# Kernel tuning notes

Hardware: AMD Instinct MI355X
Metric: run time of the kernel (lower is better)

Reference implementation:

```python
import jax, jax.numpy as jnp
import numpy as np

N_NODES = 50000
N_EDGES = 800000
IN_DIM = 128
HIDDEN_DIMS = [128, 128]
OUT_DIM = 4
NUM_GRAPHS = 128


def setup_inputs() -> dict:
    key = jax.random.key(0)
    ks = jax.random.split(key, 12)
    inp = {
        "x": jax.random.normal(ks[0], (N_NODES, IN_DIM), dtype=jnp.float32),
        "edge_index": jax.random.randint(ks[1], (2, N_EDGES), 0, N_NODES, dtype=jnp.int64),
        "edge_attr": jax.random.uniform(ks[2], (N_EDGES,), dtype=jnp.float32),
        "edge_weight": jax.random.uniform(ks[3], (N_EDGES,), dtype=jnp.float32),
        "batch": jnp.sort(jax.random.randint(ks[4], (N_NODES,), 0, NUM_GRAPHS, dtype=jnp.int64)),
    }
    # GCNConv weights (Glorot-ish scale) and biases
    d_in = IN_DIM
    for i, d_out in enumerate(HIDDEN_DIMS):
        inp[f"W{i}"] = jax.random.normal(ks[5 + i], (d_in, d_out), dtype=jnp.float32) / np.sqrt(d_in)
        inp[f"b{i}"] = jnp.zeros((d_out,), dtype=jnp.float32)
        d_in = d_out
    # classifier: Linear(d,d) -> ReLU -> Linear(d,4)
    inp["Wc1"] = jax.random.normal(ks[8], (d_in, d_in), dtype=jnp.float32) / np.sqrt(d_in)
    inp["bc1"] = jnp.zeros((d_in,), dtype=jnp.float32)
    inp["Wc2"] = jax.random.normal(ks[9], (d_in, OUT_DIM), dtype=jnp.float32) / np.sqrt(d_in)
    inp["bc2"] = jnp.zeros((OUT_DIM,), dtype=jnp.float32)
    return inp


def _gcn_conv(x, src, dst, ew, W, b):
    # PyG GCNConv with add_self_loops=True, symmetric normalization.
    n = x.shape[0]
    loop = jnp.arange(n, dtype=src.dtype)
    s = jnp.concatenate([src, loop])
    d = jnp.concatenate([dst, loop])
    w = jnp.concatenate([ew, jnp.ones((n,), dtype=ew.dtype)])
    deg = jax.ops.segment_sum(w, d, num_segments=n)
    dinv = jnp.where(deg > 0, jax.lax.rsqrt(jnp.maximum(deg, 1e-12)), 0.0)
    norm = dinv[s] * w * dinv[d]  # [E+N]
    h = x @ W                     # [N, d_out] dense GEMM
    out = jax.ops.segment_sum(h[s] * norm[:, None], d, num_segments=n)
    return out + b


def reference(x, edge_index, edge_attr, edge_weight, batch,
              W0, b0, W1, b1, Wc1, bc1, Wc2, bc2):
    # NOTE: original code passes edge_attr into GCNConv's edge_weight slot;
    # edge_weight is unused. Dropout is identity (eval mode).
    src, dst = edge_index[0], edge_index[1]
    h = x
    for W, b in ((W0, b0), (W1, b1)):
        h = _gcn_conv(h, src, dst, edge_attr, W, b)
        h = jax.nn.relu(h)
    # global mean pool over graphs
    sums = jax.ops.segment_sum(h, batch, num_segments=NUM_GRAPHS)
    cnts = jax.ops.segment_sum(jnp.ones((h.shape[0],), h.dtype), batch, num_segments=NUM_GRAPHS)
    g = sums / jnp.maximum(cnts, 1.0)[:, None]  # [G, d]
    # classifier MLP
    g = jax.nn.relu(g @ Wc1 + bc1)
    return g @ Wc2 + bc2  # [G, 4]
```

## Files before the change

### kernel.cpp

```cpp
#include <hip/hip_runtime.h>
#include <hip/hip_fp16.h>

#define N_NODES 50000
#define N_EDGES 800000
#define DIM 128
#define NUM_GRAPHS 128
#define STRIDE 64

#define ATTR_SCALE 33554432.0f
#define ATTR_MASK  ((1ull << 40) - 1)

typedef _Float16 f16x8 __attribute__((ext_vector_type(8)));
typedef float f32x4 __attribute__((ext_vector_type(4)));


__global__ __launch_bounds__(256) void k_zero(unsigned long long* packed,
                                              float* gz, int n) {
    int i = blockIdx.x * 256 + threadIdx.x;
    if (i < n) packed[i] = 0ull;
    if (i < NUM_GRAPHS * DIM + NUM_GRAPHS) gz[i] = 0.f;
}


__global__ __launch_bounds__(256) void k_build(const int* __restrict__ src,
                                               const int* __restrict__ dst,
                                               const float* __restrict__ attr,
                                               unsigned long long* packed,
                                               unsigned int* __restrict__ epack,
                                               int E) {
    int e = blockIdx.x * 256 + threadIdx.x;
    if (e >= E) return;
    int d = dst[e];
    float a = attr[e];
    unsigned long long add =
        (1ull << 40) | (unsigned long long)(unsigned int)(a * ATTR_SCALE + 0.5f);
    unsigned long long old = atomicAdd(&packed[d], add);
    int rank = (int)(old >> 40);
    if (rank < STRIDE) {
        __half ha = __float2half_rn(a);
        unsigned short us = *reinterpret_cast<unsigned short*>(&ha);
        epack[d * STRIDE + rank] = ((unsigned int)us << 16) | (unsigned int)src[e];
    }
}


__global__ __launch_bounds__(128) void k_prep_w(const float* __restrict__ W0,
                                                const float* __restrict__ W1,
                                                _Float16* __restrict__ Wt0,
                                                _Float16* __restrict__ Wt1) {
    int b = blockIdx.x;
    const float* W = (b & 1) ? W1 : W0;
    _Float16* Wt = (b & 1) ? Wt1 : Wt0;
    int k = b >> 1;
    int nn = threadIdx.x;
    Wt[(size_t)nn * 128 + k] = (_Float16)W[(size_t)k * 128 + nn];
}


__global__ __launch_bounds__(256) void k_gemm_mfma(const float* __restrict__ A,
                                                   const _Float16* __restrict__ Wt,
                                                   const unsigned long long* __restrict__ packed,
                                                   __half* __restrict__ H, int n) {
    int tid = threadIdx.x;
    int w = tid >> 6, lane = tid & 63;
    int n15 = lane & 15, quad = lane >> 4;
    int row = blockIdx.x * 64 + w * 16 + n15;
    int rowc = row < n ? row : n - 1;
    const float4* Arow = (const float4*)(A + (size_t)rowc * DIM);

    f32x4 acc[8];
#pragma unroll
    for (int t = 0; t < 8; t++) acc[t] = (f32x4){0.f, 0.f, 0.f, 0.f};

#pragma unroll
    for (int c = 0; c < 4; c++) {
        float4 a0 = Arow[c * 8 + quad * 2];
        float4 a1 = Arow[c * 8 + quad * 2 + 1];
        f16x8 af;
        af[0] = (_Float16)a0.x; af[1] = (_Float16)a0.y;
        af[2] = (_Float16)a0.z; af[3] = (_Float16)a0.w;
        af[4] = (_Float16)a1.x; af[5] = (_Float16)a1.y;
        af[6] = (_Float16)a1.z; af[7] = (_Float16)a1.w;
#pragma unroll
        for (int t = 0; t < 8; t++) {
            f16x8 bf = *(const f16x8*)(Wt + (size_t)(t * 16 + n15) * 128 + c * 32 + quad * 8);
            acc[t] = __builtin_amdgcn_mfma_f32_16x16x32_f16(af, bf, acc[t], 0, 0, 0);
        }
    }

    int orow0 = blockIdx.x * 64 + w * 16 + quad * 4;
#pragma unroll
    for (int r = 0; r < 4; r++) {
        int orow = orow0 + r;
        if (orow < n) {
            unsigned long long pk = packed[orow];
            float dv = rsqrtf(1.0f + (float)(pk & ATTR_MASK) * (1.0f / ATTR_SCALE));
            __half* hp = H + (size_t)orow * DIM + n15;
#pragma unroll
            for (int t = 0; t < 8; t++) hp[t * 16] = __float2half_rn(acc[t][r] * dv);
        }
    }
}


__device__ __forceinline__ float2 unpack_h2(unsigned int u) {
    __half2 h = *reinterpret_cast<__half2*>(&u);
    return __half22float2(h);
}

template <bool POOL>
__global__ __launch_bounds__(256) void k_gather(const __half* __restrict__ H,
                                                const unsigned long long* __restrict__ packed,
                                                const unsigned int* __restrict__ epack,
                                                const float* __restrict__ bias,
                                                const int* __restrict__ batch,
                                                float* __restrict__ OUT,
                                                float* gsum, float* cnt, int n) {
    __shared__ float lpool[8 * 128];
    __shared__ int sg[8];

    int idx = blockIdx.x * 256 + threadIdx.x;
    int i = idx >> 5;
    int lane = idx & 31;
    int w = threadIdx.x >> 5;
    const uint2* H8 = (const uint2*)H;

    unsigned long long pk = packed[i];
    int cntE = (int)(pk >> 40);
    if (cntE > STRIDE) cntE = STRIDE;
    float dv = rsqrtf(1.0f + (float)(pk & ATTR_MASK) * (1.0f / ATTR_SCALE));

    uint2 selfraw = H8[(size_t)i * 32 + lane];
    float2 s01 = unpack_h2(selfraw.x);
    float2 s23 = unpack_h2(selfraw.y);
    float4 acc = make_float4(s01.x, s01.y, s23.x, s23.y);

    int j0 = i * STRIDE;
    int end = j0 + cntE;

    for (int j = j0; j < end; j += 8) {
        int s[8];
        float wt[8];
#pragma unroll
        for (int k = 0; k < 8; k++) {
            int jj = j + k;
            bool valid = jj < end;
            int jc = valid ? jj : (end - 1);
            unsigned int pe = epack[jc];
            s[k] = (int)(pe & 0xffffu);
            __half_raw hr;
            hr.x = (unsigned short)(pe >> 16);
            float wv = __half2float(__half(hr));
            wt[k] = valid ? wv : 0.f;
        }
        uint2 v[8];
#pragma unroll
        for (int k = 0; k < 8; k++) v[k] = H8[(size_t)s[k] * 32 + lane];
#pragma unroll
        for (int k = 0; k < 8; k++) {
            float2 f01 = unpack_h2(v[k].x);
            float2 f23 = unpack_h2(v[k].y);
            acc.x += wt[k] * f01.x;
            acc.y += wt[k] * f01.y;
            acc.z += wt[k] * f23.x;
            acc.w += wt[k] * f23.y;
        }
    }

    float4 bb = ((const float4*)bias)[lane];
    acc.x = fmaxf(acc.x * dv + bb.x, 0.f);
    acc.y = fmaxf(acc.y * dv + bb.y, 0.f);
    acc.z = fmaxf(acc.z * dv + bb.z, 0.f);
    acc.w = fmaxf(acc.w * dv + bb.w, 0.f);

    if (POOL) {
        int g = batch[i];
        if (lane == 0) sg[w] = g;
        __syncthreads();
        bool uniform = true;
#pragma unroll
        for (int k = 0; k < 8; k++) uniform = uniform && (sg[k] == sg[0]);
        if (uniform) {
            ((float4*)(lpool + w * 128))[lane] = acc;
            __syncthreads();
            int t = threadIdx.x;
            if (t < 128) {
                float s = 0.f;
#pragma unroll
                for (int k = 0; k < 8; k++) s += lpool[k * 128 + t];
                atomicAdd(&gsum[sg[0] * DIM + t], s);
            }
            if (t == 0) atomicAdd(&cnt[sg[0]], 8.0f);
        } else {
            float* o = gsum + (size_t)g * DIM + lane * 4;
            atomicAdd(o + 0, acc.x);
            atomicAdd(o + 1, acc.y);
            atomicAdd(o + 2, acc.z);
            atomicAdd(o + 3, acc.w);
            if (lane == 0) atomicAdd(&cnt[g], 1.0f);
        }
    } else {
        ((float4*)OUT)[(size_t)i * 32 + lane] = acc;
    }
}


__global__ __launch_bounds__(128) void k_classifier(const float* __restrict__ gsum,
                                                    const float* __restrict__ cnt,
                                                    const float* __restrict__ Wc1,
                                                    const float* __restrict__ bc1,
                                                    const float* __restrict__ Wc2,
                                                    const float* __restrict__ bc2,
                                                    float* __restrict__ out) {
    int g = blockIdx.x;
    int t = threadIdx.x;
    __shared__ float gv[128];
    __shared__ float hid[128];
    float inv = 1.0f / fmaxf(cnt[g], 1.0f);
    gv[t] = gsum[(size_t)g * DIM + t] * inv;
    __syncthreads();
    float acc = bc1[t];
    for (int k = 0; k < 128; k++) acc += gv[k] * Wc1[k * 128 + t];
    hid[t] = fmaxf(acc, 0.f);
    __syncthreads();
    if (t < 4) {
        float o = bc2[t];
        for (int k = 0; k < 128; k++) o += hid[k] * Wc2[k * 4 + t];
        out[g * 4 + t] = o;
    }
}


extern "C" void kernel_launch(void* const* d_in, const int* in_sizes, int n_in,
                              void* d_out, int out_size, void* d_ws, size_t ws_size,
                              hipStream_t stream) {
    const float* x     = (const float*)d_in[0];
    const int*   ei    = (const int*)d_in[1];
    const float* attr  = (const float*)d_in[2];
    const int*   batch = (const int*)d_in[4];
    const float* W0  = (const float*)d_in[5];
    const float* b0  = (const float*)d_in[6];
    const float* W1  = (const float*)d_in[7];
    const float* b1  = (const float*)d_in[8];
    const float* Wc1 = (const float*)d_in[9];
    const float* bc1 = (const float*)d_in[10];
    const float* Wc2 = (const float*)d_in[11];
    const float* bc2 = (const float*)d_in[12];
    float* out = (float*)d_out;

    char* ws = (char*)d_ws;
    __half*             bufH16 = (__half*)(ws + 0);
    float*              bufA   = (float*)(ws + 12800000);
    unsigned int*       epack  = (unsigned int*)(ws + 38400000);
    unsigned long long* packed = (unsigned long long*)(ws + 51200000);
    float*              gsum   = (float*)(ws + 51600000);
    float*              cnt    = (float*)(ws + 51665536);
    _Float16*           Wt0    = (_Float16*)(ws + 51666048);
    _Float16*           Wt1    = (_Float16*)(ws + 51698816);

    const int* src = ei;
    const int* dst = ei + N_EDGES;

    const int NB_N = (N_NODES + 255) / 256;
    const int NB_E = (N_EDGES + 255) / 256;
    const int NB_G = (N_NODES * 32 + 255) / 256;
    const int NB_M = (N_NODES + 63) / 64;

    k_zero<<<NB_N, 256, 0, stream>>>(packed, gsum, N_NODES);
    k_prep_w<<<256, 128, 0, stream>>>(W0, W1, Wt0, Wt1);
    k_build<<<NB_E, 256, 0, stream>>>(src, dst, attr, packed, epack, N_EDGES);

    k_gemm_mfma<<<NB_M, 256, 0, stream>>>(x, Wt0, packed, bufH16, N_NODES);
    k_gather<false><<<NB_G, 256, 0, stream>>>(bufH16, packed, epack, b0,
                                              batch, bufA, gsum, cnt, N_NODES);

    k_gemm_mfma<<<NB_M, 256, 0, stream>>>(bufA, Wt1, packed, bufH16, N_NODES);
    k_gather<true><<<NB_G, 256, 0, stream>>>(bufH16, packed, epack, b1,
                                             batch, nullptr, gsum, cnt, N_NODES);

    k_classifier<<<NUM_GRAPHS, 128, 0, stream>>>(gsum, cnt, Wc1, bc1, Wc2, bc2, out);
}
```

Baseline: 278.9 us.

## Store layer-1 activations in fp16, swap MFMA operands, fuse prep kernels

The layer-1 gather output is now written as fp16, and the second GEMM reads it directly with no float-to-half conversion. This halves that intermediate's traffic. The MFMA operands are swapped so each lane holds four consecutive output columns, which allows packed 8-byte half stores in place of scattered 2-byte stores. Zeroing moves to a hipMemsetAsync, and the weight transpose is folded into extra blocks of the build kernel, cutting launch count. Layer-2 input precision drops from fp32 to fp16 before the GEMM, though the GEMM already converted it to fp16, so accuracy is essentially unchanged.

```diff
diff --git a/kernel.cpp b/kernel.cpp
--- a/kernel.cpp
+++ b/kernel.cpp
@@ -14,21 +14,29 @@
 typedef float f32x4 __attribute__((ext_vector_type(4)));
 
 
-__global__ __launch_bounds__(256) void k_zero(unsigned long long* packed,
-                                              float* gz, int n) {
-    int i = blockIdx.x * 256 + threadIdx.x;
-    if (i < n) packed[i] = 0ull;
-    if (i < NUM_GRAPHS * DIM + NUM_GRAPHS) gz[i] = 0.f;
-}
-
-
 __global__ __launch_bounds__(256) void k_build(const int* __restrict__ src,
                                                const int* __restrict__ dst,
                                                const float* __restrict__ attr,
+                                               const float* __restrict__ W0,
+                                               const float* __restrict__ W1,
                                                unsigned long long* packed,
                                                unsigned int* __restrict__ epack,
-                                               int E) {
-    int e = blockIdx.x * 256 + threadIdx.x;
+                                               _Float16* __restrict__ Wt0,
+                                               _Float16* __restrict__ Wt1,
+                                               int E, int nbE) {
+    int b = blockIdx.x;
+    if (b >= nbE) {
+        int idx = (b - nbE) * 256 + threadIdx.x;
+        int m = idx >> 14;
+        int rem = idx & 16383;
+        int n = rem >> 7;
+        int k = rem & 127;
+        const float* W = m ? W1 : W0;
+        _Float16* Wt = m ? Wt1 : Wt0;
+        Wt[(size_t)n * 128 + k] = (_Float16)W[(size_t)k * 128 + n];
+        return;
+    }
+    int e = b * 256 + threadIdx.x;
     if (e >= E) return;
     int d = dst[e];
     float a = attr[e];
@@ -44,29 +52,17 @@
 }
 
 
-__global__ __launch_bounds__(128) void k_prep_w(const float* __restrict__ W0,
-                                                const float* __restrict__ W1,
-                                                _Float16* __restrict__ Wt0,
-                                                _Float16* __restrict__ Wt1) {
-    int b = blockIdx.x;
-    const float* W = (b & 1) ? W1 : W0;
-    _Float16* Wt = (b & 1) ? Wt1 : Wt0;
-    int k = b >> 1;
-    int nn = threadIdx.x;
-    Wt[(size_t)nn * 128 + k] = (_Float16)W[(size_t)k * 128 + nn];
-}
-
-
-__global__ __launch_bounds__(256) void k_gemm_mfma(const float* __restrict__ A,
+template <typename AT>
+__global__ __launch_bounds__(256) void k_gemm_mfma(const AT* __restrict__ A,
                                                    const _Float16* __restrict__ Wt,
                                                    const unsigned long long* __restrict__ packed,
                                                    __half* __restrict__ H, int n) {
     int tid = threadIdx.x;
     int w = tid >> 6, lane = tid & 63;
     int n15 = lane & 15, quad = lane >> 4;
-    int row = blockIdx.x * 64 + w * 16 + n15;
-    int rowc = row < n ? row : n - 1;
-    const float4* Arow = (const float4*)(A + (size_t)rowc * DIM);
+    int node = blockIdx.x * 64 + w * 16 + n15;
+    int nodec = node < n ? node : n - 1;
+    const AT* Arow = A + (size_t)nodec * DIM;
 
     f32x4 acc[8];
 #pragma unroll
@@ -74,30 +70,36 @@
 
 #pragma unroll
     for (int c = 0; c < 4; c++) {
-        float4 a0 = Arow[c * 8 + quad * 2];
-        float4 a1 = Arow[c * 8 + quad * 2 + 1];
-        f16x8 af;
-        af[0] = (_Float16)a0.x; af[1] = (_Float16)a0.y;
-        af[2] = (_Float16)a0.z; af[3] = (_Float16)a0.w;
-        af[4] = (_Float16)a1.x; af[5] = (_Float16)a1.y;
-        af[6] = (_Float16)a1.z; af[7] = (_Float16)a1.w;
+        f16x8 bf;
+        if constexpr (__is_same(AT, float)) {
+            float4 a0 = ((const float4*)Arow)[c * 8 + quad * 2];
+            float4 a1 = ((const float4*)Arow)[c * 8 + quad * 2 + 1];
+            bf[0] = (_Float16)a0.x; bf[1] = (_Float16)a0.y;
+            bf[2] = (_Float16)a0.z; bf[3] = (_Float16)a0.w;
+            bf[4] = (_Float16)a1.x; bf[5] = (_Float16)a1.y;
+            bf[6] = (_Float16)a1.z; bf[7] = (_Float16)a1.w;
+        } else {
+            bf = *(const f16x8*)(Arow + c * 32 + quad * 8);
+        }
 #pragma unroll
         for (int t = 0; t < 8; t++) {
-            f16x8 bf = *(const f16x8*)(Wt + (size_t)(t * 16 + n15) * 128 + c * 32 + quad * 8);
+            f16x8 af = *(const f16x8*)(Wt + (size_t)(t * 16 + n15) * 128 + c * 32 + quad * 8);
             acc[t] = __builtin_amdgcn_mfma_f32_16x16x32_f16(af, bf, acc[t], 0, 0, 0);
         }
     }
 
-    int orow0 = blockIdx.x * 64 + w * 16 + quad * 4;
-#pragma unroll
-    for (int r = 0; r < 4; r++) {
-        int orow = orow0 + r;
-        if (orow < n) {
-            unsigned long long pk = packed[orow];
-            float dv = rsqrtf(1.0f + (float)(pk & ATTR_MASK) * (1.0f / ATTR_SCALE));
-            __half* hp = H + (size_t)orow * DIM + n15;
-#pragma unroll
-            for (int t = 0; t < 8; t++) hp[t * 16] = __float2half_rn(acc[t][r] * dv);
+    if (node < n) {
+        unsigned long long pk = packed[nodec];
+        float dv = rsqrtf(1.0f + (float)(pk & ATTR_MASK) * (1.0f / ATTR_SCALE));
+        __half* hp = H + (size_t)node * DIM + quad * 4;
+#pragma unroll
+        for (int t = 0; t < 8; t++) {
+            __half2 h01 = __floats2half2_rn(acc[t][0] * dv, acc[t][1] * dv);
+            __half2 h23 = __floats2half2_rn(acc[t][2] * dv, acc[t][3] * dv);
+            uint2 pkd;
+            pkd.x = *reinterpret_cast<unsigned int*>(&h01);
+            pkd.y = *reinterpret_cast<unsigned int*>(&h23);
+            *(uint2*)(hp + t * 16) = pkd;
         }
     }
 }
@@ -114,7 +116,7 @@
                                                 const unsigned int* __restrict__ epack,
                                                 const float* __restrict__ bias,
                                                 const int* __restrict__ batch,
-                                                float* __restrict__ OUT,
+                                                __half* __restrict__ OUT,
                                                 float* gsum, float* cnt, int n) {
     __shared__ float lpool[8 * 128];
     __shared__ int sg[8];
@@ -200,7 +202,12 @@
             if (lane == 0) atomicAdd(&cnt[g], 1.0f);
         }
     } else {
-        ((float4*)OUT)[(size_t)i * 32 + lane] = acc;
+        __half2 p01 = __floats2half2_rn(acc.x, acc.y);
+        __half2 p23 = __floats2half2_rn(acc.z, acc.w);
+        uint2 o;
+        o.x = *reinterpret_cast<unsigned int*>(&p01);
+        o.y = *reinterpret_cast<unsigned int*>(&p23);
+        ((uint2*)OUT)[(size_t)i * 32 + lane] = o;
     }
 }
 
@@ -250,31 +257,32 @@
 
     char* ws = (char*)d_ws;
     __half*             bufH16 = (__half*)(ws + 0);
-    float*              bufA   = (float*)(ws + 12800000);
-    unsigned int*       epack  = (unsigned int*)(ws + 38400000);
-    unsigned long long* packed = (unsigned long long*)(ws + 51200000);
-    float*              gsum   = (float*)(ws + 51600000);
-    float*              cnt    = (float*)(ws + 51665536);
-    _Float16*           Wt0    = (_Float16*)(ws + 51666048);
-    _Float16*           Wt1    = (_Float16*)(ws + 51698816);
+    __half*             bufA16 = (__half*)(ws + 12800000);
+    unsigned int*       epack  = (unsigned int*)(ws + 25600000);
+    unsigned long long* packed = (unsigned long long*)(ws + 38400000);
+    float*              gsum   = (float*)(ws + 38800000);
+    float*              cnt    = (float*)(ws + 38865536);
+    _Float16*           Wt0    = (_Float16*)(ws + 38866048);
+    _Float16*           Wt1    = (_Float16*)(ws + 38898816);
 
     const int* src = ei;
     const int* dst = ei + N_EDGES;
 
-    const int NB_N = (N_NODES + 255) / 256;
     const int NB_E = (N_EDGES + 255) / 256;
     const int NB_G = (N_NODES * 32 + 255) / 256;
     const int NB_M = (N_NODES + 63) / 64;
 
-    k_zero<<<NB_N, 256, 0, stream>>>(packed, gsum, N_NODES);
-    k_prep_w<<<256, 128, 0, stream>>>(W0, W1, Wt0, Wt1);
-    k_build<<<NB_E, 256, 0, stream>>>(src, dst, attr, packed, epack, N_EDGES);
-
-    k_gemm_mfma<<<NB_M, 256, 0, stream>>>(x, Wt0, packed, bufH16, N_NODES);
+    (void)hipMemsetAsync(ws + 38400000, 0, 466048, stream);
+
+    k_build<<<NB_E + 128, 256, 0, stream>>>(src, dst, attr, W0, W1, packed,
+                                            epack, Wt0, Wt1, N_EDGES, NB_E);
+
+    k_gemm_mfma<float><<<NB_M, 256, 0, stream>>>(x, Wt0, packed, bufH16, N_NODES);
     k_gather<false><<<NB_G, 256, 0, stream>>>(bufH16, packed, epack, b0,
-                                              batch, bufA, gsum, cnt, N_NODES);
-
-    k_gemm_mfma<<<NB_M, 256, 0, stream>>>(bufA, Wt1, packed, bufH16, N_NODES);
+                                              batch, bufA16, gsum, cnt, N_NODES);
+
+    k_gemm_mfma<_Float16><<<NB_M, 256, 0, stream>>>((const _Float16*)bufA16, Wt1,
+                                                    packed, bufH16, N_NODES);
     k_gather<true><<<NB_G, 256, 0, stream>>>(bufH16, packed, epack, b1,
                                              batch, nullptr, gsum, cnt, N_NODES);
 
```

Result: no change. 276.3 us (-0.9%).
